# Performance work log

Hardware: AMD Instinct MI355X
Metric: run time of the kernel (lower is better)

## Reference

```python
import jax, jax.numpy as jnp
import numpy as np

T, D, E, K, F, SF = 4096, 1024, 8, 2, 1024, 1024  # tokens, d_model, experts, top_k, moe_ff, shared_ff


def setup_inputs() -> dict:
    key = jax.random.key(0)
    ks = jax.random.split(key, 10)
    hidden_states = jax.random.normal(ks[0], (T, D), jnp.float32)
    # balanced expert assignment: the fused kernel's get_split_sizes assumes tokens
    # split evenly across experts after permute_tokens, so exactly T*K/E per expert
    flat = jnp.arange(T * K) % E
    flat = jax.random.permutation(ks[1], flat)
    topk_indices = flat.reshape(T, K).astype(jnp.int32)
    w = jax.random.uniform(ks[2], (T, K), jnp.float32)
    topk_weights = w / w.sum(-1, keepdims=True)  # norm_topk_prob
    s = 0.02
    w_gate = jax.random.normal(ks[3], (E, D, F), jnp.float32) * s
    w_up = jax.random.normal(ks[4], (E, D, F), jnp.float32) * s
    w_down = jax.random.normal(ks[5], (E, F, D), jnp.float32) * s
    sw_gate = jax.random.normal(ks[6], (D, SF), jnp.float32) * s
    sw_up = jax.random.normal(ks[7], (D, SF), jnp.float32) * s
    sw_down = jax.random.normal(ks[8], (SF, D), jnp.float32) * s
    shared_gate_w = jax.random.normal(ks[9], (D, 1), jnp.float32) * s
    return dict(hidden_states=hidden_states, topk_weights=topk_weights,
                w_gate=w_gate, w_up=w_up, w_down=w_down,
                sw_gate=sw_gate, sw_up=sw_up, sw_down=sw_down,
                shared_gate_w=shared_gate_w, topk_indices=topk_indices)


def _silu(x):
    return x * jax.nn.sigmoid(x)


def reference(hidden_states, topk_weights, w_gate, w_up, w_down,
              sw_gate, sw_up, sw_down, shared_gate_w, topk_indices):
    t, d = hidden_states.shape
    e = w_gate.shape[0]
    k = topk_indices.shape[1]
    c = (t * k) // e  # tokens per expert (balanced split, as in get_split_sizes)

    # permute_tokens: replicate each token top_k times and sort by expert id
    flat_idx = topk_indices.reshape(-1)                    # [t*k]
    order = jnp.argsort(flat_idx)                          # dispatch permutation
    x_rep = jnp.repeat(hidden_states, k, axis=0)           # [t*k, d]
    xs = x_rep[order].reshape(e, c, d)                     # grouped per-expert

    # per-expert gated MLP (grouped GEMMs)
    h = _silu(jnp.einsum('ecd,edf->ecf', xs, w_gate)) * jnp.einsum('ecd,edf->ecf', xs, w_up)
    y = jnp.einsum('ecf,efd->ecd', h, w_down).reshape(t * k, d)

    # unpermute_tokens + weighted combine over top_k
    y = y[jnp.argsort(order)].reshape(t, k, d)
    out = (y * topk_weights[..., None]).sum(axis=1)        # [t, d]

    # shared expert with sigmoid gate
    s = jnp.einsum('tf,fd->td', _silu(hidden_states @ sw_gate) * (hidden_states @ sw_up), sw_down)
    g = jax.nn.sigmoid(hidden_states @ shared_gate_w)      # [t, 1]
    return (out + g * s).astype(hidden_states.dtype)
```

## Files before the change

kernel.cpp:

```cpp
#include <hip/hip_runtime.h>
#include <hip/hip_bf16.h>
#include <cstdint>
#include <cstddef>

#define TTOK 4096
#define DM   1024
#define NE   8
#define KTOP 2
#define FFD  1024
#define CPER 1024
#define MROWS 12288

typedef __attribute__((ext_vector_type(8))) short frag8;
typedef __attribute__((ext_vector_type(4))) float f32x4;

static __device__ __forceinline__ unsigned short f2bf(float f) {
  unsigned int u = __float_as_uint(f);
  u += 0x7fff + ((u >> 16) & 1);
  return (unsigned short)(u >> 16);
}
static __device__ __forceinline__ float bf2f(unsigned short u) {
  return __uint_as_float((unsigned int)u << 16);
}

static __device__ __forceinline__ void gld_lds16(const unsigned short* g, unsigned short* l) {
  __builtin_amdgcn_global_load_lds(
      (const __attribute__((address_space(1))) unsigned int*)g,
      (__attribute__((address_space(3))) unsigned int*)l,
      16, 0, 0);
}

static __device__ __forceinline__ int lds_slot(int r, int cs) {
  return r * 4 + (cs ^ ((r >> 1) & 3));
}

static __device__ __forceinline__ void stage_tile(const unsigned short* __restrict__ src,
                                                  int row0, int k0,
                                                  unsigned short* lds, int tid) {
#pragma unroll
  for (int it = 0; it < 2; ++it) {
    int seg = it * 256 + tid;
    int r = seg >> 2;
    int cs = (seg & 3) ^ ((r >> 1) & 3);
    gld_lds16(src + (size_t)(row0 + r) * 1024 + k0 + cs * 8, lds + seg * 8);
  }
}

static __device__ __forceinline__ void swizzle_xy(int& x, int& y) {
  int L = blockIdx.y * 8 + blockIdx.x;
  int xcd = L & 7;
  int s = L >> 3;
  y = xcd * 12 + s % 12;
  x = s / 12;
}

__global__ void perm_kernel(const int* __restrict__ idx, const float* __restrict__ tw,
                            int* __restrict__ cnt, int* __restrict__ rowdst,
                            int* __restrict__ inv, float* __restrict__ rowscale) {
  int i = blockIdx.x * 256 + threadIdx.x;
  int e = idx[i];
  int pos = atomicAdd(&cnt[e], 1);
  int j = e * CPER + pos;
  rowdst[j] = i >> 1;
  rowscale[j] = tw[i];
  inv[i] = j;
}

__global__ void pack_gate_kernel(const float* __restrict__ x, const int* __restrict__ rowdst,
                                 const float* __restrict__ gw,
                                 float* __restrict__ rowscale,
                                 unsigned short* __restrict__ xall) {
  int j = blockIdx.x;
  int tid = threadIdx.x;
  int t = (j < 8192) ? rowdst[j] : (j - 8192);
  float4 v = ((const float4*)(x + (size_t)t * 1024))[tid];
  ushort4 o;
  o.x = f2bf(v.x); o.y = f2bf(v.y); o.z = f2bf(v.z); o.w = f2bf(v.w);
  ((ushort4*)(xall + (size_t)j * 1024))[tid] = o;
  if (j >= 8192) {
    float4 g = ((const float4*)gw)[tid];
    float s = v.x * g.x + v.y * g.y + v.z * g.z + v.w * g.w;
#pragma unroll
    for (int off = 32; off; off >>= 1) s += __shfl_down(s, off);
    __shared__ float ws[4];
    if ((tid & 63) == 0) ws[tid >> 6] = s;
    __syncthreads();
    if (tid == 0) {
      float tot = ws[0] + ws[1] + ws[2] + ws[3];
      rowscale[j] = 1.f / (1.f + __expf(-tot));
    }
  }
}

__global__ void transw_kernel(const float* __restrict__ wg, const float* __restrict__ wu,
                              const float* __restrict__ wd, const float* __restrict__ sg,
                              const float* __restrict__ su, const float* __restrict__ sd,
                              unsigned short* __restrict__ owg, unsigned short* __restrict__ owu,
                              unsigned short* __restrict__ owd) {
  int z = blockIdx.z;
  const float* src; unsigned short* dst;
  if (z < 8)       { src = wg + (size_t)z * 1048576;        dst = owg + (size_t)z * 1048576; }
  else if (z < 16) { src = wu + (size_t)(z - 8) * 1048576;  dst = owu + (size_t)(z - 8) * 1048576; }
  else if (z < 24) { src = wd + (size_t)(z - 16) * 1048576; dst = owd + (size_t)(z - 16) * 1048576; }
  else if (z == 24){ src = sg; dst = owg + (size_t)8 * 1048576; }
  else if (z == 25){ src = su; dst = owu + (size_t)8 * 1048576; }
  else             { src = sd; dst = owd + (size_t)8 * 1048576; }
  __shared__ float tile[64][65];
  int bx = blockIdx.x * 64;
  int by = blockIdx.y * 64;
  int c4 = threadIdx.x & 15;
  int r0 = threadIdx.x >> 4;
#pragma unroll
  for (int i = 0; i < 4; ++i) {
    int r = r0 + 16 * i;
    float4 v = *(const float4*)&src[(size_t)(by + r) * 1024 + bx + c4 * 4];
    tile[r][c4 * 4 + 0] = v.x; tile[r][c4 * 4 + 1] = v.y;
    tile[r][c4 * 4 + 2] = v.z; tile[r][c4 * 4 + 3] = v.w;
  }
  __syncthreads();
#pragma unroll
  for (int i = 0; i < 4; ++i) {
    int f = r0 + 16 * i;
    ushort4 o;
    o.x = f2bf(tile[c4 * 4 + 0][f]);
    o.y = f2bf(tile[c4 * 4 + 1][f]);
    o.z = f2bf(tile[c4 * 4 + 2][f]);
    o.w = f2bf(tile[c4 * 4 + 3][f]);
    *(ushort4*)&dst[(size_t)(bx + f) * 1024 + by + c4 * 4] = o;
  }
}

static __device__ __forceinline__ int eid_of(int y) { return (y < 64) ? (y >> 3) : 8; }

__global__ __launch_bounds__(256, 2) void gemm1_kernel(
    const unsigned short* __restrict__ A, const unsigned short* __restrict__ Bg,
    const unsigned short* __restrict__ Bu, unsigned short* __restrict__ H) {
  __shared__ __align__(16) unsigned short As[128 * 32];
  __shared__ __align__(16) unsigned short Bgs[128 * 32];
  __shared__ __align__(16) unsigned short Bus[128 * 32];
  int tid = threadIdx.x;
  int bx, by;
  swizzle_xy(bx, by);
  int e = eid_of(by);
  int row0 = by * 128;
  int col0 = bx * 128;
  const unsigned short* Bge = Bg + (size_t)e * 1048576;
  const unsigned short* Bue = Bu + (size_t)e * 1048576;

  int wave = tid >> 6, lane = tid & 63;
  int wm = wave >> 1, wn = wave & 1;
  int lr = lane & 15, q = lane >> 4;

  f32x4 accg[4][4], accu[4][4];
#pragma unroll
  for (int i = 0; i < 4; ++i)
#pragma unroll
    for (int j = 0; j < 4; ++j) {
      accg[i][j] = (f32x4){0.f, 0.f, 0.f, 0.f};
      accu[i][j] = (f32x4){0.f, 0.f, 0.f, 0.f};
    }

  for (int kt = 0; kt < 1024; kt += 32) {
    stage_tile(A, row0, kt, As, tid);
    stage_tile(Bge, col0, kt, Bgs, tid);
    stage_tile(Bue, col0, kt, Bus, tid);
    __syncthreads();
    frag8 a[4], b0[4], b1[4];
#pragma unroll
    for (int i = 0; i < 4; ++i) {
      int r = wm * 64 + i * 16 + lr;
      a[i] = *(const frag8*)&As[lds_slot(r, q) * 8];
    }
#pragma unroll
    for (int j = 0; j < 4; ++j) {
      int r = wn * 64 + j * 16 + lr;
      b0[j] = *(const frag8*)&Bgs[lds_slot(r, q) * 8];
      b1[j] = *(const frag8*)&Bus[lds_slot(r, q) * 8];
    }
#pragma unroll
    for (int i = 0; i < 4; ++i)
#pragma unroll
      for (int j = 0; j < 4; ++j) {
        accg[i][j] = __builtin_amdgcn_mfma_f32_16x16x32_bf16(a[i], b0[j], accg[i][j], 0, 0, 0);
        accu[i][j] = __builtin_amdgcn_mfma_f32_16x16x32_bf16(a[i], b1[j], accu[i][j], 0, 0, 0);
      }
    __syncthreads();
  }
#pragma unroll
  for (int i = 0; i < 4; ++i)
#pragma unroll
    for (int j = 0; j < 4; ++j)
#pragma unroll
      for (int r = 0; r < 4; ++r) {
        int m = row0 + wm * 64 + i * 16 + q * 4 + r;
        int n = col0 + wn * 64 + j * 16 + lr;
        float gv = accg[i][j][r];
        float hv = gv / (1.f + __expf(-gv)) * accu[i][j][r];
        H[(size_t)m * 1024 + n] = f2bf(hv);
      }
}

__global__ __launch_bounds__(256, 2) void gemm2_kernel(
    const unsigned short* __restrict__ A, const unsigned short* __restrict__ B,
    const float* __restrict__ rowscale, unsigned short* __restrict__ Y) {
  __shared__ __align__(16) unsigned short As[128 * 32];
  __shared__ __align__(16) unsigned short Bs[128 * 32];
  int tid = threadIdx.x;
  int bx, by;
  swizzle_xy(bx, by);
  int e = eid_of(by);
  int row0 = by * 128;
  int col0 = bx * 128;
  const unsigned short* Be = B + (size_t)e * 1048576;

  int wave = tid >> 6, lane = tid & 63;
  int wm = wave >> 1, wn = wave & 1;
  int lr = lane & 15, q = lane >> 4;

  f32x4 acc[4][4];
#pragma unroll
  for (int i = 0; i < 4; ++i)
#pragma unroll
    for (int j = 0; j < 4; ++j) acc[i][j] = (f32x4){0.f, 0.f, 0.f, 0.f};

  for (int kt = 0; kt < 1024; kt += 32) {
    stage_tile(A, row0, kt, As, tid);
    stage_tile(Be, col0, kt, Bs, tid);
    __syncthreads();
    frag8 a[4], b[4];
#pragma unroll
    for (int i = 0; i < 4; ++i) {
      int r = wm * 64 + i * 16 + lr;
      a[i] = *(const frag8*)&As[lds_slot(r, q) * 8];
    }
#pragma unroll
    for (int j = 0; j < 4; ++j) {
      int r = wn * 64 + j * 16 + lr;
      b[j] = *(const frag8*)&Bs[lds_slot(r, q) * 8];
    }
#pragma unroll
    for (int i = 0; i < 4; ++i)
#pragma unroll
      for (int j = 0; j < 4; ++j)
        acc[i][j] = __builtin_amdgcn_mfma_f32_16x16x32_bf16(a[i], b[j], acc[i][j], 0, 0, 0);
    __syncthreads();
  }
#pragma unroll
  for (int i = 0; i < 4; ++i)
#pragma unroll
    for (int r = 0; r < 4; ++r) {
      int m = row0 + wm * 64 + i * 16 + q * 4 + r;
      float sc = rowscale[m];
#pragma unroll
      for (int j = 0; j < 4; ++j) {
        int n = col0 + wn * 64 + j * 16 + lr;
        Y[(size_t)m * 1024 + n] = f2bf(sc * acc[i][j][r]);
      }
    }
}

__global__ void combine_kernel(const unsigned short* __restrict__ Y,
                               const int* __restrict__ inv, float* __restrict__ out) {
  int t = blockIdx.x;
  int c = threadIdx.x;
  int j0 = inv[2 * t], j1 = inv[2 * t + 1];
  ushort4 a = ((const ushort4*)(Y + (size_t)j0 * 1024))[c];
  ushort4 b = ((const ushort4*)(Y + (size_t)j1 * 1024))[c];
  ushort4 s = ((const ushort4*)(Y + (size_t)(8192 + t) * 1024))[c];
  float4 o;
  o.x = bf2f(a.x) + bf2f(b.x) + bf2f(s.x);
  o.y = bf2f(a.y) + bf2f(b.y) + bf2f(s.y);
  o.z = bf2f(a.z) + bf2f(b.z) + bf2f(s.z);
  o.w = bf2f(a.w) + bf2f(b.w) + bf2f(s.w);
  ((float4*)(out + (size_t)t * 1024))[c] = o;
}

extern "C" void kernel_launch(void* const* d_in, const int* in_sizes, int n_in,
                              void* d_out, int out_size, void* d_ws, size_t ws_size,
                              hipStream_t stream) {
  (void)in_sizes; (void)n_in; (void)out_size; (void)ws_size;
  const float* hidden  = (const float*)d_in[0];
  const float* topk_w  = (const float*)d_in[1];
  const float* w_gate  = (const float*)d_in[2];
  const float* w_up    = (const float*)d_in[3];
  const float* w_down  = (const float*)d_in[4];
  const float* sw_gate = (const float*)d_in[5];
  const float* sw_up   = (const float*)d_in[6];
  const float* sw_down = (const float*)d_in[7];
  const float* sgw     = (const float*)d_in[8];
  const int*   topk_i  = (const int*)d_in[9];
  float* out = (float*)d_out;

  char* p = (char*)d_ws;
  auto alloc = [&](size_t bytes) {
    char* r = p;
    p += (bytes + 255) & ~(size_t)255;
    return r;
  };
  unsigned short* Wg_all = (unsigned short*)alloc((size_t)9 * 1048576 * 2);
  unsigned short* Wu_all = (unsigned short*)alloc((size_t)9 * 1048576 * 2);
  unsigned short* Wd_all = (unsigned short*)alloc((size_t)9 * 1048576 * 2);
  unsigned short* Xall   = (unsigned short*)alloc((size_t)MROWS * 1024 * 2);
  unsigned short* Hall   = (unsigned short*)alloc((size_t)MROWS * 1024 * 2);
  int*   cnt      = (int*)alloc(NE * 4);
  int*   rowdst   = (int*)alloc((size_t)TTOK * KTOP * 4);
  int*   inv      = (int*)alloc((size_t)TTOK * KTOP * 4);
  float* rowscale = (float*)alloc((size_t)MROWS * 4);
  unsigned short* Yall = Xall;

  hipMemsetAsync(cnt, 0, NE * 4, stream);

  perm_kernel<<<TTOK * KTOP / 256, 256, 0, stream>>>(topk_i, topk_w, cnt, rowdst, inv, rowscale);
  pack_gate_kernel<<<MROWS, 256, 0, stream>>>(hidden, rowdst, sgw, rowscale, Xall);
  transw_kernel<<<dim3(16, 16, 27), 256, 0, stream>>>(
      w_gate, w_up, w_down, sw_gate, sw_up, sw_down, Wg_all, Wu_all, Wd_all);

  gemm1_kernel<<<dim3(8, 96), 256, 0, stream>>>(Xall, Wg_all, Wu_all, Hall);
  gemm2_kernel<<<dim3(8, 96), 256, 0, stream>>>(Hall, Wd_all, rowscale, Yall);
  combine_kernel<<<TTOK, 256, 0, stream>>>(Yall, inv, out);
}
```

Before: 318.9 us.

## Gather token rows inside gemm1 instead of materializing permuted bf16 activations

Replaces the pack kernel, which wrote a permuted and replicated 12288-row bf16 activation buffer, with a conversion that writes only 4096 bf16 token rows and computes the shared-expert sigmoid gate using one wave per row. gemm1 now gathers A rows through a per-row source index loaded once per thread, so the permutation becomes an indirect load. Combine is relaunched with fewer blocks, each handling two slots, and Y gets its own buffer instead of aliasing X. This removes about 16 MB of writes and reads of duplicated activations, at the cost of non-contiguous row gathers in gemm1.

```diff
diff --git a/kernel.cpp b/kernel.cpp
--- a/kernel.cpp
+++ b/kernel.cpp
@@ -55,41 +55,40 @@
 }
 
 __global__ void perm_kernel(const int* __restrict__ idx, const float* __restrict__ tw,
-                            int* __restrict__ cnt, int* __restrict__ rowdst,
+                            int* __restrict__ cnt, int* __restrict__ rowsrc,
                             int* __restrict__ inv, float* __restrict__ rowscale) {
   int i = blockIdx.x * 256 + threadIdx.x;
   int e = idx[i];
   int pos = atomicAdd(&cnt[e], 1);
   int j = e * CPER + pos;
-  rowdst[j] = i >> 1;
+  rowsrc[j] = i >> 1;
   rowscale[j] = tw[i];
   inv[i] = j;
-}
-
-__global__ void pack_gate_kernel(const float* __restrict__ x, const int* __restrict__ rowdst,
-                                 const float* __restrict__ gw,
+  if (i < TTOK) rowsrc[8192 + i] = i;
+}
+
+__global__ void conv_gate_kernel(const float* __restrict__ x, const float* __restrict__ gw,
                                  float* __restrict__ rowscale,
-                                 unsigned short* __restrict__ xall) {
-  int j = blockIdx.x;
-  int tid = threadIdx.x;
-  int t = (j < 8192) ? rowdst[j] : (j - 8192);
-  float4 v = ((const float4*)(x + (size_t)t * 1024))[tid];
-  ushort4 o;
-  o.x = f2bf(v.x); o.y = f2bf(v.y); o.z = f2bf(v.z); o.w = f2bf(v.w);
-  ((ushort4*)(xall + (size_t)j * 1024))[tid] = o;
-  if (j >= 8192) {
-    float4 g = ((const float4*)gw)[tid];
-    float s = v.x * g.x + v.y * g.y + v.z * g.z + v.w * g.w;
-#pragma unroll
-    for (int off = 32; off; off >>= 1) s += __shfl_down(s, off);
-    __shared__ float ws[4];
-    if ((tid & 63) == 0) ws[tid >> 6] = s;
-    __syncthreads();
-    if (tid == 0) {
-      float tot = ws[0] + ws[1] + ws[2] + ws[3];
-      rowscale[j] = 1.f / (1.f + __expf(-tot));
-    }
-  }
+                                 unsigned short* __restrict__ xb) {
+  int row = blockIdx.x * 4 + (threadIdx.x >> 6);
+  int lane = threadIdx.x & 63;
+  const float4* xr = (const float4*)(x + (size_t)row * 1024);
+  const float4* wr = (const float4*)gw;
+  ushort4* ob = (ushort4*)(xb + (size_t)row * 1024);
+  float s = 0.f;
+#pragma unroll
+  for (int c = 0; c < 4; ++c) {
+    int k = lane + 64 * c;
+    float4 v = xr[k];
+    float4 g = wr[k];
+    s += v.x * g.x + v.y * g.y + v.z * g.z + v.w * g.w;
+    ushort4 o;
+    o.x = f2bf(v.x); o.y = f2bf(v.y); o.z = f2bf(v.z); o.w = f2bf(v.w);
+    ob[k] = o;
+  }
+#pragma unroll
+  for (int off = 32; off; off >>= 1) s += __shfl_down(s, off);
+  if (lane == 0) rowscale[8192 + row] = 1.f / (1.f + __expf(-s));
 }
 
 __global__ void transw_kernel(const float* __restrict__ wg, const float* __restrict__ wu,
@@ -133,8 +132,9 @@
 static __device__ __forceinline__ int eid_of(int y) { return (y < 64) ? (y >> 3) : 8; }
 
 __global__ __launch_bounds__(256, 2) void gemm1_kernel(
-    const unsigned short* __restrict__ A, const unsigned short* __restrict__ Bg,
-    const unsigned short* __restrict__ Bu, unsigned short* __restrict__ H) {
+    const unsigned short* __restrict__ A, const int* __restrict__ rowsrc,
+    const unsigned short* __restrict__ Bg, const unsigned short* __restrict__ Bu,
+    unsigned short* __restrict__ H) {
   __shared__ __align__(16) unsigned short As[128 * 32];
   __shared__ __align__(16) unsigned short Bgs[128 * 32];
   __shared__ __align__(16) unsigned short Bus[128 * 32];
@@ -147,6 +147,13 @@
   const unsigned short* Bge = Bg + (size_t)e * 1048576;
   const unsigned short* Bue = Bu + (size_t)e * 1048576;
 
+  int sA0 = tid, sA1 = 256 + tid;
+  int rA0 = sA0 >> 2, rA1 = sA1 >> 2;
+  int cA0 = (sA0 & 3) ^ ((rA0 >> 1) & 3);
+  int cA1 = (sA1 & 3) ^ ((rA1 >> 1) & 3);
+  const unsigned short* pA0 = A + (size_t)rowsrc[row0 + rA0] * 1024 + cA0 * 8;
+  const unsigned short* pA1 = A + (size_t)rowsrc[row0 + rA1] * 1024 + cA1 * 8;
+
   int wave = tid >> 6, lane = tid & 63;
   int wm = wave >> 1, wn = wave & 1;
   int lr = lane & 15, q = lane >> 4;
@@ -161,7 +168,8 @@
     }
 
   for (int kt = 0; kt < 1024; kt += 32) {
-    stage_tile(A, row0, kt, As, tid);
+    gld_lds16(pA0 + kt, As + sA0 * 8);
+    gld_lds16(pA1 + kt, As + sA1 * 8);
     stage_tile(Bge, col0, kt, Bgs, tid);
     stage_tile(Bue, col0, kt, Bus, tid);
     __syncthreads();
@@ -261,18 +269,23 @@
 
 __global__ void combine_kernel(const unsigned short* __restrict__ Y,
                                const int* __restrict__ inv, float* __restrict__ out) {
-  int t = blockIdx.x;
-  int c = threadIdx.x;
-  int j0 = inv[2 * t], j1 = inv[2 * t + 1];
-  ushort4 a = ((const ushort4*)(Y + (size_t)j0 * 1024))[c];
-  ushort4 b = ((const ushort4*)(Y + (size_t)j1 * 1024))[c];
-  ushort4 s = ((const ushort4*)(Y + (size_t)(8192 + t) * 1024))[c];
-  float4 o;
-  o.x = bf2f(a.x) + bf2f(b.x) + bf2f(s.x);
-  o.y = bf2f(a.y) + bf2f(b.y) + bf2f(s.y);
-  o.z = bf2f(a.z) + bf2f(b.z) + bf2f(s.z);
-  o.w = bf2f(a.w) + bf2f(b.w) + bf2f(s.w);
-  ((float4*)(out + (size_t)t * 1024))[c] = o;
+  int base = blockIdx.x * 256 + threadIdx.x;
+#pragma unroll
+  for (int k = 0; k < 2; ++k) {
+    int slot = base + k * 524288;
+    int t = slot >> 8;
+    int c = slot & 255;
+    int j0 = inv[2 * t], j1 = inv[2 * t + 1];
+    ushort4 a = ((const ushort4*)(Y + (size_t)j0 * 1024))[c];
+    ushort4 b = ((const ushort4*)(Y + (size_t)j1 * 1024))[c];
+    ushort4 s = ((const ushort4*)(Y + (size_t)(8192 + t) * 1024))[c];
+    float4 o;
+    o.x = bf2f(a.x) + bf2f(b.x) + bf2f(s.x);
+    o.y = bf2f(a.y) + bf2f(b.y) + bf2f(s.y);
+    o.z = bf2f(a.z) + bf2f(b.z) + bf2f(s.z);
+    o.w = bf2f(a.w) + bf2f(b.w) + bf2f(s.w);
+    ((float4*)(out + (size_t)t * 1024))[c] = o;
+  }
 }
 
 extern "C" void kernel_launch(void* const* d_in, const int* in_sizes, int n_in,
@@ -300,22 +313,22 @@
   unsigned short* Wg_all = (unsigned short*)alloc((size_t)9 * 1048576 * 2);
   unsigned short* Wu_all = (unsigned short*)alloc((size_t)9 * 1048576 * 2);
   unsigned short* Wd_all = (unsigned short*)alloc((size_t)9 * 1048576 * 2);
-  unsigned short* Xall   = (unsigned short*)alloc((size_t)MROWS * 1024 * 2);
+  unsigned short* Xbf    = (unsigned short*)alloc((size_t)TTOK * 1024 * 2);
   unsigned short* Hall   = (unsigned short*)alloc((size_t)MROWS * 1024 * 2);
+  unsigned short* Yall   = (unsigned short*)alloc((size_t)MROWS * 1024 * 2);
   int*   cnt      = (int*)alloc(NE * 4);
-  int*   rowdst   = (int*)alloc((size_t)TTOK * KTOP * 4);
+  int*   rowsrc   = (int*)alloc((size_t)MROWS * 4);
   int*   inv      = (int*)alloc((size_t)TTOK * KTOP * 4);
   float* rowscale = (float*)alloc((size_t)MROWS * 4);
-  unsigned short* Yall = Xall;
 
   hipMemsetAsync(cnt, 0, NE * 4, stream);
 
-  perm_kernel<<<TTOK * KTOP / 256, 256, 0, stream>>>(topk_i, topk_w, cnt, rowdst, inv, rowscale);
-  pack_gate_kernel<<<MROWS, 256, 0, stream>>>(hidden, rowdst, sgw, rowscale, Xall);
+  perm_kernel<<<TTOK * KTOP / 256, 256, 0, stream>>>(topk_i, topk_w, cnt, rowsrc, inv, rowscale);
+  conv_gate_kernel<<<TTOK / 4, 256, 0, stream>>>(hidden, sgw, rowscale, Xbf);
   transw_kernel<<<dim3(16, 16, 27), 256, 0, stream>>>(
       w_gate, w_up, w_down, sw_gate, sw_up, sw_down, Wg_all, Wu_all, Wd_all);
 
-  gemm1_kernel<<<dim3(8, 96), 256, 0, stream>>>(Xall, Wg_all, Wu_all, Hall);
+  gemm1_kernel<<<dim3(8, 96), 256, 0, stream>>>(Xbf, rowsrc, Wg_all, Wu_all, Hall);
   gemm2_kernel<<<dim3(8, 96), 256, 0, stream>>>(Hall, Wd_all, rowscale, Yall);
-  combine_kernel<<<TTOK, 256, 0, stream>>>(Yall, inv, out);
-}
+  combine_kernel<<<2048, 256, 0, stream>>>(Yall, inv, out);
+}
```

After: 312.3 us. 1.02x faster.
